# Kernel optimization log

Hardware: AMD Instinct MI355X
Metric: run time of the kernel (lower is better)

Reference implementation:

```python
import jax, jax.numpy as jnp
import numpy as np

B, S = 32, 8192
HE, HD = 256, 256  # encoder_hidden_size, decoder_hidden_size


def setup_inputs() -> dict:
    key = jax.random.key(0)
    ks = jax.random.split(key, 8)
    scale = 1.0 / np.sqrt(HD)
    scale_e = 1.0 / np.sqrt(HE)
    return {
        "query": jax.random.normal(ks[0], (B, 1, HD), dtype=jnp.float32),
        "keys": jax.random.normal(ks[1], (B, S, HE), dtype=jnp.float32),
        "Wa_w": jax.random.uniform(ks[2], (HD, HD), jnp.float32, -scale, scale),
        "Wa_b": jax.random.uniform(ks[3], (HD,), jnp.float32, -scale, scale),
        "Ua_w": jax.random.uniform(ks[4], (HD, HE), jnp.float32, -scale_e, scale_e),
        "Ua_b": jax.random.uniform(ks[5], (HD,), jnp.float32, -scale_e, scale_e),
        "Va_w": jax.random.uniform(ks[6], (1, HD), jnp.float32, -scale, scale),
        "Va_b": jax.random.uniform(ks[7], (1,), jnp.float32, -scale, scale),
    }


def reference(query, keys, Wa_w, Wa_b, Ua_w, Ua_b, Va_w, Va_b):
    # q_proj: [B, 1, HD]; k_proj: [B, S, HD]
    q_proj = jnp.einsum("bqd,hd->bqh", query, Wa_w) + Wa_b
    k_proj = jnp.einsum("bse,he->bsh", keys, Ua_w) + Ua_b
    # scores: [B, S] -> [B, 1, S]
    scores = jnp.einsum("bsh,h->bs", jnp.tanh(q_proj + k_proj), Va_w[0]) + Va_b[0]
    weights = jax.nn.softmax(scores, axis=-1)[:, None, :]  # [B, 1, S]
    context = jnp.einsum("bqs,bse->bqe", weights, keys)    # [B, 1, HE]
    return (context, weights)
```

## Files before the change

### kernel.cpp

```cpp
#include <hip/hip_runtime.h>
#include <hip/hip_bf16.h>
#include <stdint.h>

#define B_ 32
#define S_ 8192
#define HD_ 256
#define HE_ 256
#define CHUNK 512
#define ROWS 16
#define MSTEPS (CHUNK/ROWS)
#define NCHUNK (S_/CHUNK)
#define TILE (ROWS * 512)

typedef __attribute__((ext_vector_type(8))) short bf16x8;
typedef __attribute__((ext_vector_type(4))) float f32x4;

__device__ __forceinline__ uint32_t cvt_pk_bf16(float lo, float hi) {
  uint32_t r;
  asm("v_cvt_pk_bf16_f32 %0, %1, %2" : "=v"(r) : "v"(lo), "v"(hi));
  return r;
}
__device__ __forceinline__ float bf2f(unsigned short h) {
  return __uint_as_float(((uint32_t)h) << 16);
}
__device__ __forceinline__ float tanh_fast(float x) {
  float e = __expf(2.0f * x);
  return 1.0f - 2.0f * __builtin_amdgcn_rcpf(e + 1.0f);
}
template<int CTRL>
__device__ __forceinline__ float dpp_shr_add(float v) {
  int t = __builtin_amdgcn_update_dpp(0, __float_as_int(v), CTRL, 0xf, 0xf, true);
  return v + __int_as_float(t);
}
__device__ __forceinline__ float row16_sum(float v) {
  v = dpp_shr_add<0x118>(v);
  v = dpp_shr_add<0x114>(v);
  v = dpp_shr_add<0x112>(v);
  v = dpp_shr_add<0x111>(v);
  return v;
}

__global__ void prep_kernel(const float* __restrict__ query,
                            const float* __restrict__ Wa_w,
                            const float* __restrict__ Wa_b,
                            const float* __restrict__ Ua_w,
                            const float* __restrict__ Ua_b,
                            float* __restrict__ qv,
                            unsigned short* __restrict__ ua_bf) {
  const int blk = blockIdx.x, t = threadIdx.x;
  if (blk < B_) {
    __shared__ float qs[HD_];
    qs[t] = query[blk * HD_ + t];
    __syncthreads();
    const float* wr = Wa_w + (size_t)t * HD_;
    float s = Wa_b[t] + Ua_b[t];
#pragma unroll 8
    for (int d = 0; d < HD_; ++d) s += qs[d] * wr[d];
    qv[blk * HD_ + t] = s;
  } else {
    const int base = (blk - B_) * 2048 + t * 8;
    float4 v0 = *(const float4*)(Ua_w + base);
    float4 v1 = *(const float4*)(Ua_w + base + 4);
    uint4 pk;
    pk.x = cvt_pk_bf16(v0.x, v0.y);
    pk.y = cvt_pk_bf16(v0.z, v0.w);
    pk.z = cvt_pk_bf16(v1.x, v1.y);
    pk.w = cvt_pk_bf16(v1.z, v1.w);
    *(uint4*)(ua_bf + base) = pk;
  }
}

__global__ __launch_bounds__(512)
__attribute__((amdgpu_waves_per_eu(4, 4)))
void main_kernel(const float* __restrict__ keys,
                 const float* __restrict__ qv,
                 const float* __restrict__ Va_w,
                 const unsigned short* __restrict__ ua_bf,
                 float* __restrict__ wexp_g,
                 float* __restrict__ partials) {
  __shared__ __align__(16) char kt[4 * TILE];
  __shared__ float sc3[3][16];
  __shared__ float wexp_l[CHUNK];
  __shared__ __align__(16) float num_l[8][64][4];

  const int t = threadIdx.x;
  const int b = blockIdx.y;
  const int chunk = blockIdx.x;
  const int s0 = chunk * CHUNK;
  const int lane = t & 63;
  const int w = t >> 6;
  const int ln = lane & 15;
  const int hi = lane >> 4;

  const unsigned short* ub0 = ua_bf + (size_t)(w * 32 + ln) * HE_ + hi * 8;
  const unsigned short* ub1 = ub0 + 16 * HE_;
  bf16x8 bb0[8], bb1[8];
#pragma unroll
  for (int k = 0; k < 8; ++k) {
    bb0[k] = *(const bf16x8*)(ub0 + k * 32);
    bb1[k] = *(const bf16x8*)(ub1 + k * 32);
  }
  const float q0  = qv[b * HD_ + w * 32 + ln];
  const float q1  = qv[b * HD_ + w * 32 + 16 + ln];
  const float va0 = Va_w[w * 32 + ln];
  const float va1 = Va_w[w * 32 + 16 + ln];

  const int srow = t >> 5;
  const int scch = t & 31;
  const float* ksrc = keys + ((size_t)b * S_ + s0 + srow) * HE_ + scch * 8;
  const int ldsoff = srow * 512 + ((scch * 16) ^ ((srow & 7) << 4));

  if (t < 48) ((float*)sc3)[t] = 0.f;
  {
    float4 a0 = *(const float4*)(ksrc);
    float4 a1 = *(const float4*)(ksrc + 4);
    uint4 pk;
    pk.x = cvt_pk_bf16(a0.x, a0.y);
    pk.y = cvt_pk_bf16(a0.z, a0.w);
    pk.z = cvt_pk_bf16(a1.x, a1.y);
    pk.w = cvt_pk_bf16(a1.z, a1.w);
    *(uint4*)(kt + ldsoff) = pk;
  }
  __syncthreads();

  const int asw = (ln & 7) << 4;
  const int nsw = (w & 7) << 4;
  float num4[4] = {0.f, 0.f, 0.f, 0.f};

  for (int i = 0; i < MSTEPS; ++i) {
    char* cur = kt + (i & 3) * TILE;
    char* stg = kt + ((i + 1) & 3) * TILE;
    char* prv = kt + ((i + 3) & 3) * TILE;

    float4 ga0, ga1;
    if (i + 1 < MSTEPS) {
      const float* kA = ksrc + (size_t)(i + 1) * ROWS * HE_;
      ga0 = *(const float4*)(kA);
      ga1 = *(const float4*)(kA + 4);
    }

    f32x4 a00 = {0.f,0.f,0.f,0.f}, a01 = {0.f,0.f,0.f,0.f};
    const char* arow = cur + ln * 512;
#pragma unroll
    for (int k = 0; k < 8; ++k) {
      bf16x8 af = *(const bf16x8*)(arow + ((k * 64 + hi * 16) ^ asw));
      a00 = __builtin_amdgcn_mfma_f32_16x16x32_bf16(af, bb0[k], a00, 0, 0, 0);
      a01 = __builtin_amdgcn_mfma_f32_16x16x32_bf16(af, bb1[k], a01, 0, 0, 0);
    }

    if (i > 0) {
      const float* scp = sc3[(i + 2) % 3];
      const float e0 = __expf(scp[w]);
      const float e8 = __expf(scp[w + 8]);
      if (lane == 0) {
        wexp_l[(i - 1) * ROWS + w] = e0;
        wexp_l[(i - 1) * ROWS + 8 + w] = e8;
      }
      uint2 kv0 = *(const uint2*)(prv + w * 512 + ((lane * 8) ^ nsw));
      uint2 kv1 = *(const uint2*)(prv + (w + 8) * 512 + ((lane * 8) ^ nsw));
      num4[0] += e0 * bf2f((unsigned short)(kv0.x & 0xffff)) + e8 * bf2f((unsigned short)(kv1.x & 0xffff));
      num4[1] += e0 * bf2f((unsigned short)(kv0.x >> 16))    + e8 * bf2f((unsigned short)(kv1.x >> 16));
      num4[2] += e0 * bf2f((unsigned short)(kv0.y & 0xffff)) + e8 * bf2f((unsigned short)(kv1.y & 0xffff));
      num4[3] += e0 * bf2f((unsigned short)(kv0.y >> 16))    + e8 * bf2f((unsigned short)(kv1.y >> 16));
    }

#pragma unroll
    for (int r = 0; r < 4; ++r) {
      float v = tanh_fast(a00[r] + q0) * va0 + tanh_fast(a01[r] + q1) * va1;
      v = row16_sum(v);
      if (ln == 15) atomicAdd(&sc3[i % 3][hi * 4 + r], v);
    }

    if (t < 16) sc3[(i + 1) % 3][t] = 0.f;

    if (i + 1 < MSTEPS) {
      uint4 pk;
      pk.x = cvt_pk_bf16(ga0.x, ga0.y);
      pk.y = cvt_pk_bf16(ga0.z, ga0.w);
      pk.z = cvt_pk_bf16(ga1.x, ga1.y);
      pk.w = cvt_pk_bf16(ga1.z, ga1.w);
      *(uint4*)(stg + ldsoff) = pk;
    }
    __syncthreads();
  }

  {
    const float* scp = sc3[(MSTEPS - 1) % 3];
    const char* prv = kt + ((MSTEPS - 1) & 3) * TILE;
    const float e0 = __expf(scp[w]);
    const float e8 = __expf(scp[w + 8]);
    if (lane == 0) {
      wexp_l[(MSTEPS - 1) * ROWS + w] = e0;
      wexp_l[(MSTEPS - 1) * ROWS + 8 + w] = e8;
    }
    uint2 kv0 = *(const uint2*)(prv + w * 512 + ((lane * 8) ^ nsw));
    uint2 kv1 = *(const uint2*)(prv + (w + 8) * 512 + ((lane * 8) ^ nsw));
    num4[0] += e0 * bf2f((unsigned short)(kv0.x & 0xffff)) + e8 * bf2f((unsigned short)(kv1.x & 0xffff));
    num4[1] += e0 * bf2f((unsigned short)(kv0.x >> 16))    + e8 * bf2f((unsigned short)(kv1.x >> 16));
    num4[2] += e0 * bf2f((unsigned short)(kv0.y & 0xffff)) + e8 * bf2f((unsigned short)(kv1.y & 0xffff));
    num4[3] += e0 * bf2f((unsigned short)(kv0.y >> 16))    + e8 * bf2f((unsigned short)(kv1.y >> 16));
  }

  *(float4*)&num_l[w][lane][0] = make_float4(num4[0], num4[1], num4[2], num4[3]);
  __syncthreads();
  wexp_g[(size_t)b * S_ + s0 + t] = wexp_l[t];
  if (t < 256) {
    float s = 0.f;
#pragma unroll
    for (int ww = 0; ww < 8; ++ww) s += num_l[ww][t >> 2][t & 3];
    partials[((size_t)b * NCHUNK + chunk) * 256 + t] = s;
  }
}

__global__ void combine_kernel(const float* __restrict__ wexp_g,
                               const float* __restrict__ partials,
                               float* __restrict__ out) {
  __shared__ float red[4];
  __shared__ float rdsh;
  const int b = blockIdx.x, t = threadIdx.x;
  const float* we = wexp_g + (size_t)b * S_;
  float s = 0.f;
#pragma unroll 4
  for (int i = t; i < S_; i += 256) s += we[i];
#pragma unroll
  for (int mm = 32; mm; mm >>= 1) s += __shfl_xor(s, mm, 64);
  if ((t & 63) == 0) red[t >> 6] = s;
  __syncthreads();
  if (t == 0) rdsh = 1.0f / (red[0] + red[1] + red[2] + red[3]);
  __syncthreads();
  const float rd = rdsh;

  const float* pb = partials + (size_t)b * NCHUNK * 256;
  float num = 0.f;
#pragma unroll 4
  for (int i = 0; i < NCHUNK; ++i) num += pb[i * 256 + t];
  out[b * HE_ + t] = num * rd;

  float* wout = out + B_ * HE_ + (size_t)b * S_;
#pragma unroll 4
  for (int i = t; i < S_; i += 256) wout[i] = we[i] * rd;
}

extern "C" void kernel_launch(void* const* d_in, const int* in_sizes, int n_in,
                              void* d_out, int out_size, void* d_ws, size_t ws_size,
                              hipStream_t stream) {
  const float* query = (const float*)d_in[0];
  const float* keys  = (const float*)d_in[1];
  const float* Wa_w  = (const float*)d_in[2];
  const float* Wa_b  = (const float*)d_in[3];
  const float* Ua_w  = (const float*)d_in[4];
  const float* Ua_b  = (const float*)d_in[5];
  const float* Va_w  = (const float*)d_in[6];
  float* out = (float*)d_out;

  char* ws = (char*)d_ws;
  float* qv             = (float*)ws;
  unsigned short* ua_bf = (unsigned short*)(ws + 32 * 1024);
  float* wexp_g         = (float*)(ws + 160 * 1024);
  float* partials       = (float*)(ws + 160 * 1024 + 1048576);

  prep_kernel<<<64, 256, 0, stream>>>(query, Wa_w, Wa_b, Ua_w, Ua_b, qv, ua_bf);
  dim3 g(NCHUNK, B_);
  main_kernel<<<g, 512, 0, stream>>>(keys, qv, Va_w, ua_bf, wexp_g, partials);
  combine_kernel<<<B_, 256, 0, stream>>>(wexp_g, partials, out);
}
```

Before: 76.12 us.

## Process two 16-row tiles per barrier with six-slot LDS ring

The main loop now handles two key tiles per iteration with one __syncthreads instead of one per tile. The LDS tile ring and score buffers grow from 4/3 slots to 6 to keep the compute, staging and previous-tile slots apart across the paired steps. This halves the number of block barriers, at the cost of more LDS (48KB of tiles) and a longer unrolled body that may raise register pressure.

```diff
diff --git a/kernel.cpp b/kernel.cpp
--- a/kernel.cpp
+++ b/kernel.cpp
@@ -9,6 +9,7 @@
 #define CHUNK 512
 #define ROWS 16
 #define MSTEPS (CHUNK/ROWS)
+#define NITER (MSTEPS/2)
 #define NCHUNK (S_/CHUNK)
 #define TILE (ROWS * 512)
 
@@ -78,8 +79,8 @@
                  const unsigned short* __restrict__ ua_bf,
                  float* __restrict__ wexp_g,
                  float* __restrict__ partials) {
-  __shared__ __align__(16) char kt[4 * TILE];
-  __shared__ float sc3[3][16];
+  __shared__ __align__(16) char kt[6 * TILE];
+  __shared__ float sc6[6][16];
   __shared__ float wexp_l[CHUNK];
   __shared__ __align__(16) float num_l[8][64][4];
 
@@ -110,88 +111,147 @@
   const float* ksrc = keys + ((size_t)b * S_ + s0 + srow) * HE_ + scch * 8;
   const int ldsoff = srow * 512 + ((scch * 16) ^ ((srow & 7) << 4));
 
-  if (t < 48) ((float*)sc3)[t] = 0.f;
-  {
-    float4 a0 = *(const float4*)(ksrc);
-    float4 a1 = *(const float4*)(ksrc + 4);
+  if (t < 96) ((float*)sc6)[t] = 0.f;
+#pragma unroll
+  for (int tl = 0; tl < 2; ++tl) {
+    const float* kA = ksrc + (size_t)tl * ROWS * HE_;
+    float4 a0 = *(const float4*)(kA);
+    float4 a1 = *(const float4*)(kA + 4);
     uint4 pk;
     pk.x = cvt_pk_bf16(a0.x, a0.y);
     pk.y = cvt_pk_bf16(a0.z, a0.w);
     pk.z = cvt_pk_bf16(a1.x, a1.y);
     pk.w = cvt_pk_bf16(a1.z, a1.w);
-    *(uint4*)(kt + ldsoff) = pk;
+    *(uint4*)(kt + tl * TILE + ldsoff) = pk;
   }
   __syncthreads();
 
   const int asw = (ln & 7) << 4;
   const int nsw = (w & 7) << 4;
   float num4[4] = {0.f, 0.f, 0.f, 0.f};
-
-  for (int i = 0; i < MSTEPS; ++i) {
-    char* cur = kt + (i & 3) * TILE;
-    char* stg = kt + ((i + 1) & 3) * TILE;
-    char* prv = kt + ((i + 3) & 3) * TILE;
+  int base = 0;
+
+  for (int j = 0; j < NITER; ++j) {
+    const int s_cur0 = base;
+    const int s_cur1 = base + 1;
+    int s_stg0 = base + 2; if (s_stg0 >= 6) s_stg0 -= 6;
+    int s_stg1 = base + 3; if (s_stg1 >= 6) s_stg1 -= 6;
+    int s_prv0 = base + 4; if (s_prv0 >= 6) s_prv0 -= 6;
+    int s_prv1 = base + 5; if (s_prv1 >= 6) s_prv1 -= 6;
+    const int i0 = 2 * j;
 
     float4 ga0, ga1;
-    if (i + 1 < MSTEPS) {
-      const float* kA = ksrc + (size_t)(i + 1) * ROWS * HE_;
+    if (i0 + 2 < MSTEPS) {
+      const float* kA = ksrc + (size_t)(i0 + 2) * ROWS * HE_;
       ga0 = *(const float4*)(kA);
       ga1 = *(const float4*)(kA + 4);
     }
 
-    f32x4 a00 = {0.f,0.f,0.f,0.f}, a01 = {0.f,0.f,0.f,0.f};
-    const char* arow = cur + ln * 512;
-#pragma unroll
-    for (int k = 0; k < 8; ++k) {
-      bf16x8 af = *(const bf16x8*)(arow + ((k * 64 + hi * 16) ^ asw));
-      a00 = __builtin_amdgcn_mfma_f32_16x16x32_bf16(af, bb0[k], a00, 0, 0, 0);
-      a01 = __builtin_amdgcn_mfma_f32_16x16x32_bf16(af, bb1[k], a01, 0, 0, 0);
-    }
-
-    if (i > 0) {
-      const float* scp = sc3[(i + 2) % 3];
-      const float e0 = __expf(scp[w]);
-      const float e8 = __expf(scp[w + 8]);
-      if (lane == 0) {
-        wexp_l[(i - 1) * ROWS + w] = e0;
-        wexp_l[(i - 1) * ROWS + 8 + w] = e8;
-      }
-      uint2 kv0 = *(const uint2*)(prv + w * 512 + ((lane * 8) ^ nsw));
-      uint2 kv1 = *(const uint2*)(prv + (w + 8) * 512 + ((lane * 8) ^ nsw));
-      num4[0] += e0 * bf2f((unsigned short)(kv0.x & 0xffff)) + e8 * bf2f((unsigned short)(kv1.x & 0xffff));
-      num4[1] += e0 * bf2f((unsigned short)(kv0.x >> 16))    + e8 * bf2f((unsigned short)(kv1.x >> 16));
-      num4[2] += e0 * bf2f((unsigned short)(kv0.y & 0xffff)) + e8 * bf2f((unsigned short)(kv1.y & 0xffff));
-      num4[3] += e0 * bf2f((unsigned short)(kv0.y >> 16))    + e8 * bf2f((unsigned short)(kv1.y >> 16));
-    }
-
-#pragma unroll
-    for (int r = 0; r < 4; ++r) {
-      float v = tanh_fast(a00[r] + q0) * va0 + tanh_fast(a01[r] + q1) * va1;
-      v = row16_sum(v);
-      if (ln == 15) atomicAdd(&sc3[i % 3][hi * 4 + r], v);
-    }
-
-    if (t < 16) sc3[(i + 1) % 3][t] = 0.f;
-
-    if (i + 1 < MSTEPS) {
-      uint4 pk;
-      pk.x = cvt_pk_bf16(ga0.x, ga0.y);
-      pk.y = cvt_pk_bf16(ga0.z, ga0.w);
-      pk.z = cvt_pk_bf16(ga1.x, ga1.y);
-      pk.w = cvt_pk_bf16(ga1.z, ga1.w);
-      *(uint4*)(stg + ldsoff) = pk;
-    }
+    {
+      f32x4 a00 = {0.f,0.f,0.f,0.f}, a01 = {0.f,0.f,0.f,0.f};
+      const char* arow = kt + s_cur0 * TILE + ln * 512;
+#pragma unroll
+      for (int k = 0; k < 8; ++k) {
+        bf16x8 af = *(const bf16x8*)(arow + ((k * 64 + hi * 16) ^ asw));
+        a00 = __builtin_amdgcn_mfma_f32_16x16x32_bf16(af, bb0[k], a00, 0, 0, 0);
+        a01 = __builtin_amdgcn_mfma_f32_16x16x32_bf16(af, bb1[k], a01, 0, 0, 0);
+      }
+      if (j > 0) {
+        const float* scp = sc6[s_prv0];
+        const char* prv = kt + s_prv0 * TILE;
+        const float e0 = __expf(scp[w]);
+        const float e8 = __expf(scp[w + 8]);
+        if (lane == 0) {
+          wexp_l[(i0 - 2) * ROWS + w] = e0;
+          wexp_l[(i0 - 2) * ROWS + 8 + w] = e8;
+        }
+        uint2 kv0 = *(const uint2*)(prv + w * 512 + ((lane * 8) ^ nsw));
+        uint2 kv1 = *(const uint2*)(prv + (w + 8) * 512 + ((lane * 8) ^ nsw));
+        num4[0] += e0 * bf2f((unsigned short)(kv0.x & 0xffff)) + e8 * bf2f((unsigned short)(kv1.x & 0xffff));
+        num4[1] += e0 * bf2f((unsigned short)(kv0.x >> 16))    + e8 * bf2f((unsigned short)(kv1.x >> 16));
+        num4[2] += e0 * bf2f((unsigned short)(kv0.y & 0xffff)) + e8 * bf2f((unsigned short)(kv1.y & 0xffff));
+        num4[3] += e0 * bf2f((unsigned short)(kv0.y >> 16))    + e8 * bf2f((unsigned short)(kv1.y >> 16));
+      }
+#pragma unroll
+      for (int r = 0; r < 4; ++r) {
+        float v = tanh_fast(a00[r] + q0) * va0 + tanh_fast(a01[r] + q1) * va1;
+        v = row16_sum(v);
+        if (ln == 15) atomicAdd(&sc6[s_cur0][hi * 4 + r], v);
+      }
+      if (i0 + 2 < MSTEPS) {
+        uint4 pk;
+        pk.x = cvt_pk_bf16(ga0.x, ga0.y);
+        pk.y = cvt_pk_bf16(ga0.z, ga0.w);
+        pk.z = cvt_pk_bf16(ga1.x, ga1.y);
+        pk.w = cvt_pk_bf16(ga1.z, ga1.w);
+        *(uint4*)(kt + s_stg0 * TILE + ldsoff) = pk;
+      }
+    }
+
+    if (i0 + 3 < MSTEPS) {
+      const float* kA = ksrc + (size_t)(i0 + 3) * ROWS * HE_;
+      ga0 = *(const float4*)(kA);
+      ga1 = *(const float4*)(kA + 4);
+    }
+
+    {
+      f32x4 a00 = {0.f,0.f,0.f,0.f}, a01 = {0.f,0.f,0.f,0.f};
+      const char* arow = kt + s_cur1 * TILE + ln * 512;
+#pragma unroll
+      for (int k = 0; k < 8; ++k) {
+        bf16x8 af = *(const bf16x8*)(arow + ((k * 64 + hi * 16) ^ asw));
+        a00 = __builtin_amdgcn_mfma_f32_16x16x32_bf16(af, bb0[k], a00, 0, 0, 0);
+        a01 = __builtin_amdgcn_mfma_f32_16x16x32_bf16(af, bb1[k], a01, 0, 0, 0);
+      }
+      if (j > 0) {
+        const float* scp = sc6[s_prv1];
+        const char* prv = kt + s_prv1 * TILE;
+        const float e0 = __expf(scp[w]);
+        const float e8 = __expf(scp[w + 8]);
+        if (lane == 0) {
+          wexp_l[(i0 - 1) * ROWS + w] = e0;
+          wexp_l[(i0 - 1) * ROWS + 8 + w] = e8;
+        }
+        uint2 kv0 = *(const uint2*)(prv + w * 512 + ((lane * 8) ^ nsw));
+        uint2 kv1 = *(const uint2*)(prv + (w + 8) * 512 + ((lane * 8) ^ nsw));
+        num4[0] += e0 * bf2f((unsigned short)(kv0.x & 0xffff)) + e8 * bf2f((unsigned short)(kv1.x & 0xffff));
+        num4[1] += e0 * bf2f((unsigned short)(kv0.x >> 16))    + e8 * bf2f((unsigned short)(kv1.x >> 16));
+        num4[2] += e0 * bf2f((unsigned short)(kv0.y & 0xffff)) + e8 * bf2f((unsigned short)(kv1.y & 0xffff));
+        num4[3] += e0 * bf2f((unsigned short)(kv0.y >> 16))    + e8 * bf2f((unsigned short)(kv1.y >> 16));
+      }
+#pragma unroll
+      for (int r = 0; r < 4; ++r) {
+        float v = tanh_fast(a00[r] + q0) * va0 + tanh_fast(a01[r] + q1) * va1;
+        v = row16_sum(v);
+        if (ln == 15) atomicAdd(&sc6[s_cur1][hi * 4 + r], v);
+      }
+      if (t < 16) sc6[s_stg0][t] = 0.f;
+      else if (t < 32) sc6[s_stg1][t - 16] = 0.f;
+      if (i0 + 3 < MSTEPS) {
+        uint4 pk;
+        pk.x = cvt_pk_bf16(ga0.x, ga0.y);
+        pk.y = cvt_pk_bf16(ga0.z, ga0.w);
+        pk.z = cvt_pk_bf16(ga1.x, ga1.y);
+        pk.w = cvt_pk_bf16(ga1.z, ga1.w);
+        *(uint4*)(kt + s_stg1 * TILE + ldsoff) = pk;
+      }
+    }
+
+    base += 2; if (base >= 6) base -= 6;
     __syncthreads();
   }
 
-  {
-    const float* scp = sc3[(MSTEPS - 1) % 3];
-    const char* prv = kt + ((MSTEPS - 1) & 3) * TILE;
+#pragma unroll
+  for (int f = 0; f < 2; ++f) {
+    const int tl = MSTEPS - 2 + f;
+    const int slot = tl % 6;
+    const float* scp = sc6[slot];
+    const char* prv = kt + slot * TILE;
     const float e0 = __expf(scp[w]);
     const float e8 = __expf(scp[w + 8]);
     if (lane == 0) {
-      wexp_l[(MSTEPS - 1) * ROWS + w] = e0;
-      wexp_l[(MSTEPS - 1) * ROWS + 8 + w] = e8;
+      wexp_l[tl * ROWS + w] = e0;
+      wexp_l[tl * ROWS + 8 + w] = e8;
     }
     uint2 kv0 = *(const uint2*)(prv + w * 512 + ((lane * 8) ^ nsw));
     uint2 kv1 = *(const uint2*)(prv + (w + 8) * 512 + ((lane * 8) ^ nsw));
```

After: 77.99 us. 1.02x slower.
